# Optimization experiments

Hardware: AMD Instinct MI355X
Metric: run time of the kernel (lower is better)

The kernel has to match this reference:

```python
import jax, jax.numpy as jnp
import numpy as np

N_EMBD = 1024
N_HEADS = 16
HEAD_DIM = N_EMBD // N_HEADS


def setup_inputs() -> dict:
    key = jax.random.key(0)
    k0, k1, k2, k3, k4 = jax.random.split(key, 5)
    scale = 1.0 / np.sqrt(N_EMBD)
    x = jax.random.normal(k0, (2, 2048, N_EMBD), dtype=jnp.float32)
    # nn.Linear(n_embd, 3*n_embd): weight [3d, d], bias [3d]
    w_qkv = jax.random.normal(k1, (3 * N_EMBD, N_EMBD), dtype=jnp.float32) * scale
    b_qkv = jax.random.normal(k2, (3 * N_EMBD,), dtype=jnp.float32) * scale
    w_proj = jax.random.normal(k3, (N_EMBD, N_EMBD), dtype=jnp.float32) * scale
    b_proj = jax.random.normal(k4, (N_EMBD,), dtype=jnp.float32) * scale
    return {"x": x, "w_qkv": w_qkv, "b_qkv": b_qkv, "w_proj": w_proj, "b_proj": b_proj}


def reference(x, w_qkv, b_qkv, w_proj, b_proj):
    b, l, d = x.shape
    h, f = N_HEADS, HEAD_DIM
    qkv = x @ w_qkv.T + b_qkv                      # [b, l, 3d]
    # rearrange 'b l (c h f) -> c b h l f'
    qkv = qkv.reshape(b, l, 3, h, f)
    q = jnp.transpose(qkv[:, :, 0], (0, 2, 1, 3))  # [b, h, l, f]
    k = jnp.transpose(qkv[:, :, 1], (0, 2, 1, 3))
    v = jnp.transpose(qkv[:, :, 2], (0, 2, 1, 3))
    scores = jnp.einsum('bhqf,bhkf->bhqk', q, k) / jnp.sqrt(jnp.float32(f))
    att = jax.nn.softmax(scores, axis=-1)          # [b, h, l, l]
    y = jnp.einsum('bhqk,bhkf->bhqf', att, v)      # [b, h, l, f]
    y = jnp.transpose(y, (0, 2, 1, 3)).reshape(b, l, d)  # 'b h l f -> b l (h f)'
    return y @ w_proj.T + b_proj
```

## Files before the change

kernel.cpp:

```cpp
#include <hip/hip_runtime.h>
#include <hip/hip_bf16.h>
#include <stdint.h>


typedef unsigned short u16;
typedef __attribute__((ext_vector_type(8))) short short8;
typedef __attribute__((ext_vector_type(4))) float f32x4;
typedef __attribute__((ext_vector_type(16))) float f32x16;
typedef __attribute__((ext_vector_type(4))) unsigned int u32x4;

#define MFMA16(a, b, c) __builtin_amdgcn_mfma_f32_16x16x32_bf16((a), (b), (c), 0, 0, 0)
#define MFMA32(a, b, c) __builtin_amdgcn_mfma_f32_32x32x16_bf16((a), (b), (c), 0, 0, 0)

__device__ __forceinline__ u16 f2bf(float x) {
  union { float f; uint32_t u; } v; v.f = x;
  uint32_t r = v.u + 0x7FFFu + ((v.u >> 16) & 1u);
  return (u16)(r >> 16);
}

__device__ __forceinline__ float fexp2(float x) {
#if __has_builtin(__builtin_amdgcn_exp2f)
  return __builtin_amdgcn_exp2f(x);
#else
  return exp2f(x);
#endif
}

__device__ __forceinline__ uint32_t pkbf(float lo, float hi) {
  uint32_t a = __builtin_bit_cast(uint32_t, lo) + 0x8000u;
  uint32_t b = __builtin_bit_cast(uint32_t, hi) + 0x8000u;
  return __builtin_amdgcn_perm(b, a, 0x07060302u);
}

__device__ __forceinline__ uint32_t cvtpk(float lo, float hi) {
  uint32_t r;
  asm("v_cvt_pk_bf16_f32 %0, %1, %2" : "=v"(r) : "v"(lo), "v"(hi));
  return r;
}

__device__ __forceinline__ void gload16(const void* g, void* l) {
  __builtin_amdgcn_global_load_lds((const __attribute__((address_space(1))) void*)g,
                                   (__attribute__((address_space(3))) void*)l, 16, 0, 0);
}

__global__ __launch_bounds__(256) void cvt_all(const float* __restrict__ x,
                                               const float* __restrict__ wq,
                                               const float* __restrict__ wp,
                                               u16* __restrict__ xb,
                                               u16* __restrict__ wqb,
                                               u16* __restrict__ wpb) {
  int i = blockIdx.x * 256 + threadIdx.x;
  const float* s; u16* d; int off;
  if (i < 1048576) { s = x; d = xb; off = i; }
  else if (i < 1835008) { s = wq; d = wqb; off = i - 1048576; }
  else { s = wp; d = wpb; off = i - 1835008; }
  float4 f = reinterpret_cast<const float4*>(s)[off];
  ushort4 o;
  o.x = f2bf(f.x); o.y = f2bf(f.y); o.z = f2bf(f.z); o.w = f2bf(f.w);
  reinterpret_cast<ushort4*>(d)[off] = o;
}

template <int EPI>
__global__ __launch_bounds__(256, 4) void gemm_bt(const u16* __restrict__ A,
                                                  const u16* __restrict__ B,
                                                  const float* __restrict__ bias,
                                                  u16* __restrict__ outb,
                                                  float* __restrict__ outf,
                                                  int M, int N, int K) {
  __shared__ u16 smem[16384];
  const int tid = threadIdx.x;
  const int lane = tid & 63;
  const int wid = tid >> 6;
  const int bn = blockIdx.x, bm = blockIdx.y;
  const int row0 = bm * 128, col0 = bn * 128;
  const int wr = wid >> 1, wc = wid & 1;
  const int fr = lane & 15, fq = lane >> 4;

  f32x4 acc[4][4];
  #pragma unroll
  for (int m = 0; m < 4; m++)
    #pragma unroll
    for (int n = 0; n < 4; n++)
      #pragma unroll
      for (int j = 0; j < 4; j++) acc[m][n][j] = 0.f;

  const int cB = tid + 256;
  const int rA1 = tid >> 2, rA2 = cB >> 2;
  const int lA1 = (tid & 3) ^ ((tid >> 3) & 3);
  const int lA2 = (cB & 3) ^ ((cB >> 3) & 3);
  const size_t ga1 = (size_t)rA1 * K + lA1 * 8;
  const size_t ga2 = (size_t)rA2 * K + lA2 * 8;
  const int d1 = tid * 8, d2 = cB * 8;
  const u16* Ab = A + (size_t)row0 * K;
  const u16* Bb = B + (size_t)col0 * K;

  const int sl = (fq ^ ((fr >> 1) & 3)) * 8;
  const int niter = K >> 5;

  {
    u16* s = smem;
    gload16(Ab + ga1, s + d1);
    gload16(Ab + ga2, s + d2);
    gload16(Bb + ga1, s + 4096 + d1);
    gload16(Bb + ga2, s + 4096 + d2);
  }
  __syncthreads();

  for (int t = 0; t < niter; t++) {
    if (t + 1 < niter) {
      u16* s = smem + ((t + 1) & 1) * 8192;
      const size_t k0 = (size_t)(t + 1) * 32;
      gload16(Ab + ga1 + k0, s + d1);
      gload16(Ab + ga2 + k0, s + d2);
      gload16(Bb + ga1 + k0, s + 4096 + d1);
      gload16(Bb + ga2 + k0, s + 4096 + d2);
    }
    const u16* sa = smem + (t & 1) * 8192;
    const u16* sb = sa + 4096;
    short8 a[4], b[4];
    #pragma unroll
    for (int m = 0; m < 4; m++)
      a[m] = *(const short8*)&sa[(wr * 64 + m * 16 + fr) * 32 + sl];
    #pragma unroll
    for (int n = 0; n < 4; n++)
      b[n] = *(const short8*)&sb[(wc * 64 + n * 16 + fr) * 32 + sl];
    __builtin_amdgcn_s_setprio(1);
    #pragma unroll
    for (int m = 0; m < 4; m++)
      #pragma unroll
      for (int n = 0; n < 4; n++)
        acc[m][n] = MFMA16(a[m], b[n], acc[m][n]);
    __builtin_amdgcn_s_setprio(0);
    __syncthreads();
  }

  if (EPI == 0) {
    if (bn < 16) {
      #pragma unroll
      for (int m = 0; m < 4; m++) {
        #pragma unroll
        for (int n = 0; n < 4; n++) {
          #pragma unroll
          for (int j = 0; j < 4; j++) {
            int r = row0 + wr * 64 + m * 16 + fq * 4 + j;
            int c = col0 + wc * 64 + n * 16 + fr;
            float v = acc[m][n][j] + bias[c];
            int d = c & 1023, h = d >> 6, f = d & 63;
            int bb = r >> 11, ll = r & 2047;
            int bhh = bb * 16 + h;
            if (bn < 8) {
              outb[((size_t)bhh * 2048 + ll) * 64 + f] = f2bf(v * 0.18033688f);
            } else {
              outb[4194304u + ((size_t)bhh * 2048 + ll) * 64 + f] = f2bf(v);
            }
          }
        }
      }
    } else {
      u16* sC = smem;
      #pragma unroll
      for (int m = 0; m < 4; m++) {
        #pragma unroll
        for (int n = 0; n < 4; n++) {
          int c_local = wc * 64 + n * 16 + fr;
          int r_base = wr * 64 + m * 16 + fq * 4;
          float bi = bias[col0 + c_local];
          uint2 w;
          w.x = pkbf(acc[m][n][0] + bi, acc[m][n][1] + bi);
          w.y = pkbf(acc[m][n][2] + bi, acc[m][n][3] + bi);
          *(uint2*)&sC[c_local * 128 + (r_base ^ ((c_local & 7) << 3))] = w;
        }
      }
      __syncthreads();
      const int h0 = (col0 - 2048) >> 6;
      const int ll0 = row0 & 2047;
      const int bb = row0 >> 11;
      #pragma unroll
      for (int it = 0; it < 8; it++) {
        int chunk = tid + it * 256;
        int row_c = chunk >> 4, off = chunk & 15;
        short8 v = *(const short8*)&sC[row_c * 128 + ((off * 8) ^ ((row_c & 7) << 3))];
        int h = h0 + (row_c >> 6), f = row_c & 63;
        *(short8*)&outb[8388608u + ((size_t)((bb * 16 + h) * 64 + f)) * 2048 + ll0 + off * 8] = v;
      }
    }
  } else {
    #pragma unroll
    for (int m = 0; m < 4; m++)
      #pragma unroll
      for (int n = 0; n < 4; n++)
        #pragma unroll
        for (int j = 0; j < 4; j++) {
          int r = row0 + wr * 64 + m * 16 + fq * 4 + j;
          int c = col0 + wc * 64 + n * 16 + fr;
          outf[(size_t)r * N + c] = acc[m][n][j] + bias[c];
        }
  }
}

__device__ __forceinline__ void softpack1(const f32x16& st, float& lp,
                                          short8& paA, short8& paB) {
  float e[16];
  #pragma unroll
  for (int r = 0; r < 16; r++) e[r] = fexp2(st[r]);
  float s0 = (e[0] + e[1]) + (e[2] + e[3]);
  float s1 = (e[4] + e[5]) + (e[6] + e[7]);
  float s2 = (e[8] + e[9]) + (e[10] + e[11]);
  float s3 = (e[12] + e[13]) + (e[14] + e[15]);
  lp += (s0 + s1) + (s2 + s3);
  #pragma unroll
  for (int cc = 0; cc < 2; cc++) {
    uint32_t g0 = cvtpk(e[8 * cc + 0], e[8 * cc + 1]);
    uint32_t g1 = cvtpk(e[8 * cc + 2], e[8 * cc + 3]);
    uint32_t g2 = cvtpk(e[8 * cc + 4], e[8 * cc + 5]);
    uint32_t g3 = cvtpk(e[8 * cc + 6], e[8 * cc + 7]);
    asm volatile("v_permlane32_swap_b32 %0, %1" : "+v"(g0), "+v"(g2));
    asm volatile("v_permlane32_swap_b32 %0, %1" : "+v"(g1), "+v"(g3));
    u32x4 t;
    t[0] = g0; t[1] = g1; t[2] = g2; t[3] = g3;
    if (cc == 0) paA = __builtin_bit_cast(short8, t);
    else paB = __builtin_bit_cast(short8, t);
  }
}

__global__ __launch_bounds__(256, 4) void attn_kernel(const u16* __restrict__ qg,
                                                      const u16* __restrict__ kg,
                                                      const u16* __restrict__ vtg,
                                                      u16* __restrict__ y) {
  __shared__ u16 sStage[16384];
  __shared__ float sL2[64];
  const int x = blockIdx.x;
  const int bh = (x & 7) * 4 + (x >> 8);
  const int qt = (x >> 3) & 31;
  const int tid = threadIdx.x, l = tid & 63, wid = tid >> 6;
  const int qs = wid & 1, kh = wid >> 1;
  const int col = l & 31, hi = l >> 5;
  const size_t base = (size_t)bh * 131072;
  const u16* qp = qg + base;
  const int qrow = qt * 64 + qs * 32;

  short8 qf[4];
  #pragma unroll
  for (int kk = 0; kk < 4; kk++)
    qf[kk] = *(const short8*)&qp[(size_t)(qrow + col) * 64 + kk * 16 + hi * 8];

  const int kc_src = (tid >> 3) * 64 + (((tid & 7) ^ ((tid >> 3) & 7)) * 8);
  const int vc_src = (tid >> 2) * 2048 + (((tid & 3) ^ ((tid >> 3) & 3)) * 8);
  const int kdst = tid * 8;
  const int vdst = 2048 + tid * 8;
  u16* R0 = sStage;
  u16* R1 = sStage + 8192;
  const u16* kp0 = kg + base;
  const u16* kp1 = kg + base + 65536;
  const u16* vp0 = vtg + base;
  const u16* vp1 = vtg + base + 1024;

  f32x16 o0, o1, zv;
  float lp = 0.f;
  #pragma unroll
  for (int r = 0; r < 16; r++) { o0[r] = 0.f; o1[r] = 0.f; zv[r] = 0.f; }

  const int krsw = (col & 7) << 3;
  const int vrsw = ((col >> 1) & 3) << 3;
  const u16* Rw = sStage + kh * 8192;

  gload16(kp0 + kc_src, R0 + kdst);
  gload16(vp0 + vc_src, R0 + vdst);
  gload16(kp1 + kc_src, R1 + kdst);
  gload16(vp1 + vc_src, R1 + vdst);

  int sel = 0;
  for (int t = 0; t < 32; t++) {
    __syncthreads();
    if (t + 1 < 32) {
      const size_t ko = (size_t)(t + 1) * 2048;
      const int vo = (t + 1) * 32;
      u16* b0 = R0 + (sel ^ 1) * 4096;
      u16* b1 = R1 + (sel ^ 1) * 4096;
      gload16(kp0 + ko + kc_src, b0 + kdst);
      gload16(vp0 + vo + vc_src, b0 + vdst);
      gload16(kp1 + ko + kc_src, b1 + kdst);
      gload16(vp1 + vo + vc_src, b1 + vdst);
    }
    const u16* S = Rw + sel * 4096;

    f32x16 st;
    __builtin_amdgcn_s_setprio(1);
    {
      short8 kb = *(const short8*)&S[col * 64 + ((hi * 8) ^ krsw)];
      st = MFMA32(kb, qf[0], zv);
    }
    #pragma unroll
    for (int kk = 1; kk < 4; kk++) {
      short8 kb = *(const short8*)&S[col * 64 + ((kk * 16 + hi * 8) ^ krsw)];
      st = MFMA32(kb, qf[kk], st);
    }
    __builtin_amdgcn_s_setprio(0);

    short8 pa[2];
    softpack1(st, lp, pa[0], pa[1]);

    __builtin_amdgcn_s_setprio(1);
    #pragma unroll
    for (int c = 0; c < 2; c++) {
      short8 vb0 = *(const short8*)&S[2048 + col * 32 + ((c * 16 + hi * 8) ^ vrsw)];
      short8 vb1 = *(const short8*)&S[2048 + (32 + col) * 32 + ((c * 16 + hi * 8) ^ vrsw)];
      o0 = MFMA32(pa[c], vb0, o0);
      o1 = MFMA32(pa[c], vb1, o1);
    }
    __builtin_amdgcn_s_setprio(0);
    sel ^= 1;
  }

  __syncthreads();
  float* sM = (float*)sStage;
  float* sMl = sM + 4096;
  if (kh == 1) {
    #pragma unroll
    for (int r = 0; r < 16; r++) {
      sM[qs * 2048 + r * 64 + l] = o0[r];
      sM[qs * 2048 + (16 + r) * 64 + l] = o1[r];
    }
    sMl[qs * 64 + l] = lp;
  }
  __syncthreads();
  if (kh == 0) {
    #pragma unroll
    for (int r = 0; r < 16; r++) {
      o0[r] += sM[qs * 2048 + r * 64 + l];
      o1[r] += sM[qs * 2048 + (16 + r) * 64 + l];
    }
    lp += sMl[qs * 64 + l];
    float lsum = lp + __shfl_xor(lp, 32);
    if (l < 32) sL2[qs * 32 + col] = 1.0f / lsum;
    __builtin_amdgcn_s_waitcnt(0);
    const int b = bh >> 4, hh = bh & 15;
    #pragma unroll
    for (int fvt = 0; fvt < 2; fvt++) {
      #pragma unroll
      for (int r = 0; r < 16; r++) {
        int q = (r & 3) + 8 * (r >> 2) + 4 * hi;
        float li = sL2[qs * 32 + q];
        float v = (fvt == 0 ? o0[r] : o1[r]) * li;
        y[((size_t)(b * 2048 + qrow + q)) * 1024 + hh * 64 + fvt * 32 + col] = f2bf(v);
      }
    }
  }
}

extern "C" void kernel_launch(void* const* d_in, const int* in_sizes, int n_in,
                              void* d_out, int out_size, void* d_ws, size_t ws_size,
                              hipStream_t stream) {
  const float* x = (const float*)d_in[0];
  const float* w_qkv = (const float*)d_in[1];
  const float* b_qkv = (const float*)d_in[2];
  const float* w_proj = (const float*)d_in[3];
  const float* b_proj = (const float*)d_in[4];
  float* out = (float*)d_out;

  u16* ws = (u16*)d_ws;
  u16* xb = ws;
  u16* wq = xb + 4194304;
  u16* wp = wq + 3145728;
  u16* qb = wp + 1048576;
  u16* kb = qb + 4194304;
  u16* vb = kb + 4194304;
  u16* yb = vb + 4194304;

  cvt_all<<<8192, 256, 0, stream>>>(x, w_qkv, w_proj, xb, wq, wp);

  gemm_bt<0><<<dim3(24, 32), 256, 0, stream>>>(xb, wq, b_qkv, qb, nullptr, 4096, 3072, 1024);

  attn_kernel<<<1024, 256, 0, stream>>>(qb, kb, vb, yb);

  gemm_bt<1><<<dim3(8, 32), 256, 0, stream>>>(yb, wp, b_proj, nullptr, out, 4096, 1024, 1024);
}
```

Baseline: 119.2 us.

## Load K/V tiles directly from global into registers, dropping LDS staging

Replaces the shared-memory double-buffered K/V staging (async global-to-LDS loads plus per-tile __syncthreads) with direct per-lane global loads into registers. K fragments are software-pipelined one tile ahead in register arrays, and V fragments are loaded at the start of each tile. This removes the LDS round trip and block-wide barriers, so LDS shrinks to the reduction buffer only. In exchange, the two waves sharing a key half each load the same K/V data, uncoalesced strided V loads expose more global latency, and register pressure rises.

After: 205.8 us. +72.6%, slower.

```diff
diff --git a/kernel.cpp b/kernel.cpp
--- a/kernel.cpp
+++ b/kernel.cpp
@@ -227,7 +227,7 @@
                                                       const u16* __restrict__ kg,
                                                       const u16* __restrict__ vtg,
                                                       u16* __restrict__ y) {
-  __shared__ u16 sStage[16384];
+  __shared__ float sMbuf[4224];
   __shared__ float sL2[64];
   const int x = blockIdx.x;
   const int bh = (x & 7) * 4 + (x >> 8);
@@ -244,77 +244,54 @@
   for (int kk = 0; kk < 4; kk++)
     qf[kk] = *(const short8*)&qp[(size_t)(qrow + col) * 64 + kk * 16 + hi * 8];
 
-  const int kc_src = (tid >> 3) * 64 + (((tid & 7) ^ ((tid >> 3) & 7)) * 8);
-  const int vc_src = (tid >> 2) * 2048 + (((tid & 3) ^ ((tid >> 3) & 3)) * 8);
-  const int kdst = tid * 8;
-  const int vdst = 2048 + tid * 8;
-  u16* R0 = sStage;
-  u16* R1 = sStage + 8192;
-  const u16* kp0 = kg + base;
-  const u16* kp1 = kg + base + 65536;
-  const u16* vp0 = vtg + base;
-  const u16* vp1 = vtg + base + 1024;
+  const u16* kb0 = kg + base + (size_t)kh * 65536 + col * 64 + hi * 8;
+  const u16* vb0 = vtg + base + (size_t)kh * 1024 + (size_t)col * 2048 + hi * 8;
+  const u16* vb1 = vb0 + 32 * 2048;
 
   f32x16 o0, o1, zv;
   float lp = 0.f;
   #pragma unroll
   for (int r = 0; r < 16; r++) { o0[r] = 0.f; o1[r] = 0.f; zv[r] = 0.f; }
 
-  const int krsw = (col & 7) << 3;
-  const int vrsw = ((col >> 1) & 3) << 3;
-  const u16* Rw = sStage + kh * 8192;
-
-  gload16(kp0 + kc_src, R0 + kdst);
-  gload16(vp0 + vc_src, R0 + vdst);
-  gload16(kp1 + kc_src, R1 + kdst);
-  gload16(vp1 + vc_src, R1 + vdst);
-
-  int sel = 0;
-  for (int t = 0; t < 32; t++) {
-    __syncthreads();
+  short8 kA[4], kB[4], vc[4];
+  #pragma unroll
+  for (int kk = 0; kk < 4; kk++) kA[kk] = *(const short8*)(kb0 + kk * 16);
+
+  auto TILE = [&](short8* cur, short8* nxt, int t) {
+    vc[0] = *(const short8*)(vb0 + t * 32);
+    vc[1] = *(const short8*)(vb1 + t * 32);
+    vc[2] = *(const short8*)(vb0 + t * 32 + 16);
+    vc[3] = *(const short8*)(vb1 + t * 32 + 16);
     if (t + 1 < 32) {
-      const size_t ko = (size_t)(t + 1) * 2048;
-      const int vo = (t + 1) * 32;
-      u16* b0 = R0 + (sel ^ 1) * 4096;
-      u16* b1 = R1 + (sel ^ 1) * 4096;
-      gload16(kp0 + ko + kc_src, b0 + kdst);
-      gload16(vp0 + vo + vc_src, b0 + vdst);
-      gload16(kp1 + ko + kc_src, b1 + kdst);
-      gload16(vp1 + vo + vc_src, b1 + vdst);
-    }
-    const u16* S = Rw + sel * 4096;
-
+      #pragma unroll
+      for (int kk = 0; kk < 4; kk++)
+        nxt[kk] = *(const short8*)(kb0 + (t + 1) * 2048 + kk * 16);
+    }
     f32x16 st;
     __builtin_amdgcn_s_setprio(1);
-    {
-      short8 kb = *(const short8*)&S[col * 64 + ((hi * 8) ^ krsw)];
-      st = MFMA32(kb, qf[0], zv);
-    }
-    #pragma unroll
-    for (int kk = 1; kk < 4; kk++) {
-      short8 kb = *(const short8*)&S[col * 64 + ((kk * 16 + hi * 8) ^ krsw)];
-      st = MFMA32(kb, qf[kk], st);
-    }
+    st = MFMA32(cur[0], qf[0], zv);
+    #pragma unroll
+    for (int kk = 1; kk < 4; kk++) st = MFMA32(cur[kk], qf[kk], st);
     __builtin_amdgcn_s_setprio(0);
 
     short8 pa[2];
     softpack1(st, lp, pa[0], pa[1]);
 
     __builtin_amdgcn_s_setprio(1);
-    #pragma unroll
-    for (int c = 0; c < 2; c++) {
-      short8 vb0 = *(const short8*)&S[2048 + col * 32 + ((c * 16 + hi * 8) ^ vrsw)];
-      short8 vb1 = *(const short8*)&S[2048 + (32 + col) * 32 + ((c * 16 + hi * 8) ^ vrsw)];
-      o0 = MFMA32(pa[c], vb0, o0);
-      o1 = MFMA32(pa[c], vb1, o1);
-    }
+    o0 = MFMA32(pa[0], vc[0], o0);
+    o1 = MFMA32(pa[0], vc[1], o1);
+    o0 = MFMA32(pa[1], vc[2], o0);
+    o1 = MFMA32(pa[1], vc[3], o1);
     __builtin_amdgcn_s_setprio(0);
-    sel ^= 1;
-  }
-
-  __syncthreads();
-  float* sM = (float*)sStage;
-  float* sMl = sM + 4096;
+  };
+
+  for (int t = 0; t < 32; t += 2) {
+    TILE(kA, kB, t);
+    TILE(kB, kA, t + 1);
+  }
+
+  float* sM = sMbuf;
+  float* sMl = sMbuf + 4096;
   if (kh == 1) {
     #pragma unroll
     for (int r = 0; r < 16; r++) {
```

## Double attention block size and use triple-buffered K/V staging with single barrier

Applied to the files above, without the earlier changes.

The attention kernel now runs 512-thread blocks covering 128 query rows, so each K/V tile loaded into shared memory is reused by twice as many waves. Staging moves to a three-deep ring with explicit vmcnt waits and one barrier per iteration, and the K and V loads are split across thread halves. This is meant to cut global K/V traffic and the cost of barrier stalls. In exchange it uses more LDS per block and launches half as many blocks, which may lower occupancy. The epilogue merge and the indexing of sMl and sL2 are only partly updated in the visible code, so correctness depends on the lines not shown.

Measured after the change: 113.2 us. 5.1% less time.

```diff
diff --git a/kernel.cpp b/kernel.cpp
--- a/kernel.cpp
+++ b/kernel.cpp
@@ -223,37 +223,44 @@
   }
 }
 
-__global__ __launch_bounds__(256, 4) void attn_kernel(const u16* __restrict__ qg,
+__global__ __launch_bounds__(512, 4) void attn_kernel(const u16* __restrict__ qg,
                                                       const u16* __restrict__ kg,
                                                       const u16* __restrict__ vtg,
                                                       u16* __restrict__ y) {
-  __shared__ u16 sStage[16384];
-  __shared__ float sL2[64];
+  __shared__ u16 sStage[24576];
+  __shared__ float sL2[128];
   const int x = blockIdx.x;
-  const int bh = (x & 7) * 4 + (x >> 8);
-  const int qt = (x >> 3) & 31;
+  const int bh = (x & 7) * 4 + (x >> 7);
+  const int qt = (x >> 3) & 15;
   const int tid = threadIdx.x, l = tid & 63, wid = tid >> 6;
-  const int qs = wid & 1, kh = wid >> 1;
+  const int qs = wid & 3, kh = wid >> 2;
   const int col = l & 31, hi = l >> 5;
   const size_t base = (size_t)bh * 131072;
   const u16* qp = qg + base;
-  const int qrow = qt * 64 + qs * 32;
+  const int qrow = qt * 128 + qs * 32;
 
   short8 qf[4];
   #pragma unroll
   for (int kk = 0; kk < 4; kk++)
     qf[kk] = *(const short8*)&qp[(size_t)(qrow + col) * 64 + kk * 16 + hi * 8];
 
-  const int kc_src = (tid >> 3) * 64 + (((tid & 7) ^ ((tid >> 3) & 7)) * 8);
-  const int vc_src = (tid >> 2) * 2048 + (((tid & 3) ^ ((tid >> 3) & 3)) * 8);
-  const int kdst = tid * 8;
-  const int vdst = 2048 + tid * 8;
+  const bool isK = tid < 256;
+  int srcoff, dstoff;
+  if (isK) {
+    int cc = tid, row = cc >> 3;
+    srcoff = row * 64 + (((cc & 7) ^ (row & 7)) * 8);
+    dstoff = cc * 8;
+  } else {
+    int cv = tid - 256, row = cv >> 2;
+    srcoff = row * 2048 + (((cv & 3) ^ ((cv >> 3) & 3)) * 8);
+    dstoff = 2048 + cv * 8;
+  }
   u16* R0 = sStage;
-  u16* R1 = sStage + 8192;
-  const u16* kp0 = kg + base;
-  const u16* kp1 = kg + base + 65536;
-  const u16* vp0 = vtg + base;
-  const u16* vp1 = vtg + base + 1024;
+  u16* R1 = sStage + 12288;
+  const u16* kbase0 = kg + base;
+  const u16* kbase1 = kg + base + 65536;
+  const u16* vbase0 = vtg + base;
+  const u16* vbase1 = vtg + base + 1024;
 
   f32x16 o0, o1, zv;
   float lp = 0.f;
@@ -262,26 +269,30 @@
 
   const int krsw = (col & 7) << 3;
   const int vrsw = ((col >> 1) & 3) << 3;
-  const u16* Rw = sStage + kh * 8192;
-
-  gload16(kp0 + kc_src, R0 + kdst);
-  gload16(vp0 + vc_src, R0 + vdst);
-  gload16(kp1 + kc_src, R1 + kdst);
-  gload16(vp1 + vc_src, R1 + vdst);
-
+  const u16* Rw = sStage + kh * 12288;
+
+  auto STAGE = [&](int tt, int buf) {
+    if (isK) {
+      gload16(kbase0 + (size_t)tt * 2048 + srcoff, R0 + buf * 4096 + dstoff);
+      gload16(kbase1 + (size_t)tt * 2048 + srcoff, R1 + buf * 4096 + dstoff);
+    } else {
+      gload16(vbase0 + tt * 32 + srcoff, R0 + buf * 4096 + dstoff);
+      gload16(vbase1 + tt * 32 + srcoff, R1 + buf * 4096 + dstoff);
+    }
+  };
+
+  STAGE(0, 0);
   int sel = 0;
   for (int t = 0; t < 32; t++) {
-    __syncthreads();
+    const int nb = (sel == 2) ? 0 : sel + 1;
     if (t + 1 < 32) {
-      const size_t ko = (size_t)(t + 1) * 2048;
-      const int vo = (t + 1) * 32;
-      u16* b0 = R0 + (sel ^ 1) * 4096;
-      u16* b1 = R1 + (sel ^ 1) * 4096;
-      gload16(kp0 + ko + kc_src, b0 + kdst);
-      gload16(vp0 + vo + vc_src, b0 + vdst);
-      gload16(kp1 + ko + kc_src, b1 + kdst);
-      gload16(vp1 + vo + vc_src, b1 + vdst);
-    }
+      STAGE(t + 1, nb);
+      asm volatile("s_waitcnt vmcnt(2)" ::: "memory");
+    } else {
+      asm volatile("s_waitcnt vmcnt(0)" ::: "memory");
+    }
+    __builtin_amdgcn_s_barrier();
+    __builtin_amdgcn_sched_barrier(0);
     const u16* S = Rw + sel * 4096;
 
     f32x16 st;
@@ -309,12 +320,12 @@
       o1 = MFMA32(pa[c], vb1, o1);
     }
     __builtin_amdgcn_s_setprio(0);
-    sel ^= 1;
+    sel = nb;
   }
 
   __syncthreads();
   float* sM = (float*)sStage;
-  float* sMl = sM + 4096;
+  float* sMl = sM + 8192;
   if (kh == 1) {
     #pragma unroll
     for (int r = 0; r < 16; r++) {
@@ -371,7 +382,7 @@
 
   gemm_bt<0><<<dim3(24, 32), 256, 0, stream>>>(xb, wq, b_qkv, qb, nullptr, 4096, 3072, 1024);
 
-  attn_kernel<<<1024, 256, 0, stream>>>(qb, kb, vb, yb);
+  attn_kernel<<<512, 512, 0, stream>>>(qb, kb, vb, yb);
 
   gemm_bt<1><<<dim3(8, 32), 256, 0, stream>>>(yb, wp, b_proj, nullptr, out, 4096, 1024, 1024);
 }
```
